# Kernel tuning notes

Hardware: AMD Instinct MI355X
Metric: run time of the kernel (lower is better)

## Reference

```python
import jax, jax.numpy as jnp
import numpy as np

NUM_NEG = 100
TEMP = 0.05
EPS = 1e-12  # matches F.normalize eps


def _l2norm(x):
    n = jnp.sqrt(jnp.sum(x * x, axis=-1, keepdims=True))
    return x / jnp.maximum(n, EPS)


def setup_inputs() -> dict:
    key = jax.random.key(0)
    k1, k2, k3, k4, k5, k6 = jax.random.split(key, 6)
    B, S, D = 1024, 50, 64
    NUM_ITEMS = 100000  # table has NUM_ITEMS+1 rows (row 0 = padding)
    N = B * S
    return {
        "output_embeddings": jax.random.normal(k1, (B, S, D), dtype=jnp.float32),
        "target_ids": jax.random.randint(k2, (B, S), 1, NUM_ITEMS + 1, dtype=jnp.int64)
                      if jax.config.jax_enable_x64 else
                      jax.random.randint(k2, (B, S), 1, NUM_ITEMS + 1).astype(jnp.int32),
        "all_item_embeddings": jax.random.normal(k3, (NUM_ITEMS + 1, D), dtype=jnp.float32),
        "supervision_weights": jax.random.uniform(k4, (B, S), dtype=jnp.float32),
        "neg_indices": jax.random.randint(k5, (N, NUM_NEG), 1, NUM_ITEMS + 1).astype(jnp.int32),
        "alt_neg_indices": jax.random.randint(k6, (N, NUM_NEG), 1, NUM_ITEMS + 1).astype(jnp.int32),
    }


def reference(output_embeddings, target_ids, all_item_embeddings,
              supervision_weights, neg_indices, alt_neg_indices):
    B, S, D = output_embeddings.shape
    flat_out = output_embeddings.reshape(-1, D)            # [N, D]
    flat_tgt = target_ids.reshape(-1)                       # [N]
    flat_w = supervision_weights.reshape(-1)                # [N]
    valid = flat_w > 0

    vo = _l2norm(flat_out)                                  # [N, D]
    items = _l2norm(all_item_embeddings)                    # [V, D]

    pos_e = items[flat_tgt]                                 # [N, D]
    pos_logit = jnp.sum(vo * pos_e, axis=1)                 # [N]

    # resample negatives that collide with the positive target
    neg = jnp.where(neg_indices != flat_tgt[:, None], neg_indices, alt_neg_indices)
    neg_e = items[neg]                                      # [N, K, D]
    neg_logits = jnp.einsum('nd,nkd->nk', vo, neg_e)        # [N, K]

    logits = jnp.concatenate([pos_logit[:, None], neg_logits], axis=1) / TEMP
    # cross-entropy with label 0 == logsumexp - positive logit
    loss_per = jax.nn.logsumexp(logits, axis=1) - logits[:, 0]

    wm = jnp.where(valid, flat_w, 0.0)
    return jnp.sum(loss_per * wm) / jnp.sum(wm)
```

## Files before the change

kernel.cpp:

```cpp
#include <hip/hip_runtime.h>


#define D_DIM 64
#define K_NEG 100
#define INV_TEMP 20.0f
#define MAX_LOGIT 20.0f
#define LOG2E 1.4426950408889634f
#define LN2 0.6931471805599453f

#define NBLK_MAIN 2048
#define NBLK_NORM 512
#define NT 7

typedef float fv2 __attribute__((ext_vector_type(2)));

__global__ __launch_bounds__(256) void normalize_kernel(
    const float* __restrict__ items, unsigned int* __restrict__ tab, int V) {
  const int lane = threadIdx.x & 63;
  const int wid  = threadIdx.x >> 6;
  const int g = lane >> 4, q = lane & 15;
  const int waveId = blockIdx.x * 4 + wid;
  const int nWaves = gridDim.x * 4;
  for (int base = waveId * 4; base < V; base += nWaves * 4) {
    const int r = base + g;
    const bool act = (r < V);
    float4 x = make_float4(0.f, 0.f, 0.f, 0.f);
    if (act) x = *reinterpret_cast<const float4*>(items + (size_t)r * D_DIM + q * 4);
    float ss = x.x * x.x + x.y * x.y + x.z * x.z + x.w * x.w;
    ss += __shfl_xor(ss, 1);
    ss += __shfl_xor(ss, 2);
    ss += __shfl_xor(ss, 4);
    ss += __shfl_xor(ss, 8);
    const float inv = 1.0f / fmaxf(sqrtf(ss), 1e-12f);
    if (act) {
      int u = 0;
      u = __builtin_amdgcn_cvt_pk_fp8_f32(x.x * inv, x.y * inv, u, false);
      u = __builtin_amdgcn_cvt_pk_fp8_f32(x.z * inv, x.w * inv, u, true);
      tab[(size_t)r * 16 + q] = (unsigned int)u;
    }
  }
}

__global__ __launch_bounds__(256, 4) void loss_kernel(
    const float* __restrict__ oe,
    const int*   __restrict__ tgt,
    const unsigned int* __restrict__ tab,
    const float* __restrict__ wgt,
    const int*   __restrict__ negi,
    const int*   __restrict__ alti,
    float2*      __restrict__ partials,
    int N) {
  const int lane = threadIdx.x & 63;
  const int wid  = threadIdx.x >> 6;
  const int g = lane >> 2, q = lane & 3;
  const int waveId = blockIdx.x * 4 + wid;
  const int nWaves = gridDim.x * 4;

  float num = 0.f, den = 0.f;

  int row = waveId;
  float4 a0, a1, a2, a3;
  int t_r = 0;
  float w = 0.f;
  int nj0 = 0, nj1 = 0, nj2 = 0, nj3 = 0, nj4 = 0, nj5 = 0, nj6 = 0;

  if (row < N) {
    const float* orow = oe + (size_t)row * D_DIM + q * 16;
    a0 = *reinterpret_cast<const float4*>(orow + 0);
    a1 = *reinterpret_cast<const float4*>(orow + 4);
    a2 = *reinterpret_cast<const float4*>(orow + 8);
    a3 = *reinterpret_cast<const float4*>(orow + 12);
    t_r = tgt[row];
    w = wgt[row];
    const int* nrow = negi + (size_t)row * K_NEG;
    if (g >= 1) nj0 = nrow[g - 1];
    nj1 = nrow[16 + g - 1];
    nj2 = nrow[32 + g - 1];
    nj3 = nrow[48 + g - 1];
    nj4 = nrow[64 + g - 1];
    nj5 = nrow[80 + g - 1];
    if (g <= 4) nj6 = nrow[96 + g - 1];
  }

  while (row < N) {
    const int nxt = row + nWaves;
    const int* __restrict__ arow = alti + (size_t)row * K_NEG;

    int idx[NT];
    {
      int v0 = (g == 0) ? t_r : nj0;
      if (g >= 1 && v0 == t_r) v0 = arow[g - 1];
      idx[0] = v0;
      int v1 = nj1; if (v1 == t_r) v1 = arow[16 + g - 1]; idx[1] = v1;
      int v2 = nj2; if (v2 == t_r) v2 = arow[32 + g - 1]; idx[2] = v2;
      int v3 = nj3; if (v3 == t_r) v3 = arow[48 + g - 1]; idx[3] = v3;
      int v4 = nj4; if (v4 == t_r) v4 = arow[64 + g - 1]; idx[4] = v4;
      int v5 = nj5; if (v5 == t_r) v5 = arow[80 + g - 1]; idx[5] = v5;
      int v6 = 0;
      if (g <= 4) { v6 = nj6; if (v6 == t_r) v6 = arow[96 + g - 1]; }
      idx[6] = v6;
    }

    uint4 rb[NT];
#pragma unroll
    for (int t = 0; t < NT; ++t)
      rb[t] = *reinterpret_cast<const uint4*>(tab + (size_t)idx[t] * 16 + q * 4);

    float4 b0, b1, b2, b3;
    int p_t = 0; float p_w = 0.f;
    int pn0 = 0, pn1 = 0, pn2 = 0, pn3 = 0, pn4 = 0, pn5 = 0, pn6 = 0;
    b0 = b1 = b2 = b3 = make_float4(0.f, 0.f, 0.f, 0.f);
    if (nxt < N) {
      const float* prow = oe + (size_t)nxt * D_DIM + q * 16;
      b0 = *reinterpret_cast<const float4*>(prow + 0);
      b1 = *reinterpret_cast<const float4*>(prow + 4);
      b2 = *reinterpret_cast<const float4*>(prow + 8);
      b3 = *reinterpret_cast<const float4*>(prow + 12);
      p_t = tgt[nxt];
      p_w = wgt[nxt];
      const int* nrow = negi + (size_t)nxt * K_NEG;
      if (g >= 1) pn0 = nrow[g - 1];
      pn1 = nrow[16 + g - 1];
      pn2 = nrow[32 + g - 1];
      pn3 = nrow[48 + g - 1];
      pn4 = nrow[64 + g - 1];
      pn5 = nrow[80 + g - 1];
      if (g <= 4) pn6 = nrow[96 + g - 1];
    }

    const fv2 qa0 = {a0.x, a0.y}, qa1 = {a0.z, a0.w};
    const fv2 qa2 = {a1.x, a1.y}, qa3 = {a1.z, a1.w};
    const fv2 qa4 = {a2.x, a2.y}, qa5 = {a2.z, a2.w};
    const fv2 qa6 = {a3.x, a3.y}, qa7 = {a3.z, a3.w};

    fv2 ss2 = qa0 * qa0;
    ss2 += qa1 * qa1;
    ss2 += qa2 * qa2;
    ss2 += qa3 * qa3;
    ss2 += qa4 * qa4;
    ss2 += qa5 * qa5;
    ss2 += qa6 * qa6;
    ss2 += qa7 * qa7;
    float ss = ss2[0] + ss2[1];
    ss += __shfl_xor(ss, 1);
    ss += __shfl_xor(ss, 2);
    const float inv_o = 1.0f / fmaxf(sqrtf(ss), 1e-12f);

    float sumexp = 0.f;
    float pos_logit = 0.f;

#pragma unroll
    for (int t = 0; t < NT; ++t) {
      const uint4 r = rb[t];
      fv2 acc;
      acc  = qa0 * __builtin_amdgcn_cvt_pk_f32_fp8((int)r.x, false);
      acc += qa1 * __builtin_amdgcn_cvt_pk_f32_fp8((int)r.x, true);
      acc += qa2 * __builtin_amdgcn_cvt_pk_f32_fp8((int)r.y, false);
      acc += qa3 * __builtin_amdgcn_cvt_pk_f32_fp8((int)r.y, true);
      acc += qa4 * __builtin_amdgcn_cvt_pk_f32_fp8((int)r.z, false);
      acc += qa5 * __builtin_amdgcn_cvt_pk_f32_fp8((int)r.z, true);
      acc += qa6 * __builtin_amdgcn_cvt_pk_f32_fp8((int)r.w, false);
      acc += qa7 * __builtin_amdgcn_cvt_pk_f32_fp8((int)r.w, true);
      float p = acc[0] + acc[1];
      p += __shfl_xor(p, 1);
      p += __shfl_xor(p, 2);
      const int j = t * 16 + g;
      if (q == 0 && j <= K_NEG) {
        const float logit = p * inv_o * INV_TEMP;
        sumexp += exp2f((logit - MAX_LOGIT) * LOG2E);
        if (j == 0) pos_logit = logit;
      }
    }
    sumexp += __shfl_xor(sumexp, 4);
    sumexp += __shfl_xor(sumexp, 8);
    sumexp += __shfl_xor(sumexp, 16);
    sumexp += __shfl_xor(sumexp, 32);
    if (lane == 0) {
      const float lse = log2f(sumexp) * LN2 + MAX_LOGIT;
      const float loss = lse - pos_logit;
      if (w > 0.f) {
        num += loss * w;
        den += w;
      }
    }

    a0 = b0; a1 = b1; a2 = b2; a3 = b3;
    t_r = p_t; w = p_w;
    nj0 = pn0; nj1 = pn1; nj2 = pn2; nj3 = pn3; nj4 = pn4; nj5 = pn5; nj6 = pn6;
    row = nxt;
  }

  __shared__ float2 red[4];
  if (lane == 0) red[wid] = make_float2(num, den);
  __syncthreads();
  if (threadIdx.x == 0) {
    float n = 0.f, d = 0.f;
#pragma unroll
    for (int i = 0; i < 4; ++i) { n += red[i].x; d += red[i].y; }
    partials[blockIdx.x] = make_float2(n, d);
  }
}

__global__ __launch_bounds__(256) void finish_kernel(
    const float2* __restrict__ partials, int nblk, float* __restrict__ out) {
  float num = 0.f, den = 0.f;
  for (int i = threadIdx.x; i < nblk; i += 256) {
    const float2 p = partials[i];
    num += p.x;
    den += p.y;
  }
#pragma unroll
  for (int m = 1; m < 64; m <<= 1) {
    num += __shfl_xor(num, m);
    den += __shfl_xor(den, m);
  }
  __shared__ float2 red[4];
  const int wid = threadIdx.x >> 6;
  const int lane = threadIdx.x & 63;
  if (lane == 0) red[wid] = make_float2(num, den);
  __syncthreads();
  if (threadIdx.x == 0) {
    float n = 0.f, d = 0.f;
#pragma unroll
    for (int i = 0; i < 4; ++i) { n += red[i].x; d += red[i].y; }
    out[0] = n / d;
  }
}

extern "C" void kernel_launch(void* const* d_in, const int* in_sizes, int n_in,
                              void* d_out, int out_size, void* d_ws, size_t ws_size,
                              hipStream_t stream) {
  const float* oe    = (const float*)d_in[0];
  const int*   tgt   = (const int*)  d_in[1];
  const float* items = (const float*)d_in[2];
  const float* wgt   = (const float*)d_in[3];
  const int*   negi  = (const int*)  d_in[4];
  const int*   alti  = (const int*)  d_in[5];

  const int N = in_sizes[0] / D_DIM;
  const int V = in_sizes[2] / D_DIM;

  unsigned int* tab = (unsigned int*)d_ws;
  size_t off = ((size_t)V * 16 * sizeof(unsigned int) + 255) & ~(size_t)255;
  float2* partials = (float2*)((char*)d_ws + off);

  normalize_kernel<<<NBLK_NORM, 256, 0, stream>>>(items, tab, V);
  loss_kernel<<<NBLK_MAIN, 256, 0, stream>>>(oe, tgt, tab, wgt, negi, alti,
                                             partials, N);
  finish_kernel<<<1, 256, 0, stream>>>(partials, NBLK_MAIN, (float*)d_out);
}
```

Before: 70.75 us.

## Switch to int8 quantized embeddings with sdot4 and one-lane-per-negative mapping

Replaces the fp8 item table with symmetric int8 quantization (scale 127) and also pre-quantizes the normalized output embeddings to int8 in a combined prepass kernel. The loss kernel now gives each lane a whole negative row (two per lane, 101 candidates) and computes dot products with packed int8 sdot4, dropping per-row norm computation, fp8 conversions and intra-row shuffles. Each lane now issues 64-byte gathers, and the prepass adds a write of the quantized output embeddings. Int8 rounding of both operands changes numerical accuracy relative to the fp8 version.

```diff
diff --git a/kernel.cpp b/kernel.cpp
--- a/kernel.cpp
+++ b/kernel.cpp
@@ -7,15 +7,40 @@
 #define MAX_LOGIT 20.0f
 #define LOG2E 1.4426950408889634f
 #define LN2 0.6931471805599453f
+#define MAXL2 28.853900817779268f
+#define MCONST (INV_TEMP / (127.0f * 127.0f))
+#define MC2 (MCONST * LOG2E)
 
 #define NBLK_MAIN 2048
-#define NBLK_NORM 512
-#define NT 7
-
-typedef float fv2 __attribute__((ext_vector_type(2)));
-
-__global__ __launch_bounds__(256) void normalize_kernel(
-    const float* __restrict__ items, unsigned int* __restrict__ tab, int V) {
+#define NBLK_QNT 1024
+
+typedef float fv4 __attribute__((ext_vector_type(4)));
+typedef unsigned int uv4 __attribute__((ext_vector_type(4)));
+
+__device__ __forceinline__ int DOT4(int a, int b, int c) {
+#if __has_builtin(__builtin_amdgcn_sdot4)
+  return __builtin_amdgcn_sdot4(a, b, c, false);
+#else
+  int r = c;
+#pragma unroll
+  for (int i = 0; i < 4; ++i)
+    r += (int)(signed char)(a >> (8 * i)) * (int)(signed char)(b >> (8 * i));
+  return r;
+#endif
+}
+
+__device__ __forceinline__ unsigned int pack8(const fv4 x, float s) {
+  const int b0 = (int)rintf(x.x * s) & 255;
+  const int b1 = (int)rintf(x.y * s) & 255;
+  const int b2 = (int)rintf(x.z * s) & 255;
+  const int b3 = (int)rintf(x.w * s) & 255;
+  return (unsigned)b0 | ((unsigned)b1 << 8) | ((unsigned)b2 << 16) |
+         ((unsigned)b3 << 24);
+}
+
+__global__ __launch_bounds__(256) void quantize_kernel(
+    const float* __restrict__ items, unsigned int* __restrict__ tab8, int V,
+    const float* __restrict__ oe, unsigned int* __restrict__ q8, int N) {
   const int lane = threadIdx.x & 63;
   const int wid  = threadIdx.x >> 6;
   const int g = lane >> 4, q = lane & 15;
@@ -24,179 +49,149 @@
   for (int base = waveId * 4; base < V; base += nWaves * 4) {
     const int r = base + g;
     const bool act = (r < V);
-    float4 x = make_float4(0.f, 0.f, 0.f, 0.f);
-    if (act) x = *reinterpret_cast<const float4*>(items + (size_t)r * D_DIM + q * 4);
+    fv4 x = {0.f, 0.f, 0.f, 0.f};
+    if (act) x = *reinterpret_cast<const fv4*>(items + (size_t)r * D_DIM + q * 4);
     float ss = x.x * x.x + x.y * x.y + x.z * x.z + x.w * x.w;
     ss += __shfl_xor(ss, 1);
     ss += __shfl_xor(ss, 2);
     ss += __shfl_xor(ss, 4);
     ss += __shfl_xor(ss, 8);
-    const float inv = 1.0f / fmaxf(sqrtf(ss), 1e-12f);
-    if (act) {
-      int u = 0;
-      u = __builtin_amdgcn_cvt_pk_fp8_f32(x.x * inv, x.y * inv, u, false);
-      u = __builtin_amdgcn_cvt_pk_fp8_f32(x.z * inv, x.w * inv, u, true);
-      tab[(size_t)r * 16 + q] = (unsigned int)u;
-    }
-  }
-}
-
-__global__ __launch_bounds__(256, 4) void loss_kernel(
-    const float* __restrict__ oe,
+    const float s = 127.0f / fmaxf(sqrtf(ss), 1e-12f);
+    if (act) tab8[(size_t)r * 16 + q] = pack8(x, s);
+  }
+  for (int base = waveId * 4; base < N; base += nWaves * 4) {
+    const int r = base + g;
+    const bool act = (r < N);
+    fv4 x = {0.f, 0.f, 0.f, 0.f};
+    if (act) x = *reinterpret_cast<const fv4*>(oe + (size_t)r * D_DIM + q * 4);
+    float ss = x.x * x.x + x.y * x.y + x.z * x.z + x.w * x.w;
+    ss += __shfl_xor(ss, 1);
+    ss += __shfl_xor(ss, 2);
+    ss += __shfl_xor(ss, 4);
+    ss += __shfl_xor(ss, 8);
+    const float s = 127.0f / fmaxf(sqrtf(ss), 1e-12f);
+    if (act) q8[(size_t)r * 16 + q] = pack8(x, s);
+  }
+}
+
+__global__ __launch_bounds__(256) void loss_kernel(
+    const unsigned int* __restrict__ q8,
     const int*   __restrict__ tgt,
-    const unsigned int* __restrict__ tab,
+    const unsigned int* __restrict__ tab8,
     const float* __restrict__ wgt,
     const int*   __restrict__ negi,
     const int*   __restrict__ alti,
     float2*      __restrict__ partials,
     int N) {
+  __shared__ float2 s_red[4];
   const int lane = threadIdx.x & 63;
   const int wid  = threadIdx.x >> 6;
-  const int g = lane >> 2, q = lane & 3;
   const int waveId = blockIdx.x * 4 + wid;
   const int nWaves = gridDim.x * 4;
+  const bool v1ok = (lane <= K_NEG - 64);
 
   float num = 0.f, den = 0.f;
 
   int row = waveId;
-  float4 a0, a1, a2, a3;
-  int t_r = 0;
+  int t_r = 0, n0 = 0, n1 = 0;
   float w = 0.f;
-  int nj0 = 0, nj1 = 0, nj2 = 0, nj3 = 0, nj4 = 0, nj5 = 0, nj6 = 0;
-
   if (row < N) {
-    const float* orow = oe + (size_t)row * D_DIM + q * 16;
-    a0 = *reinterpret_cast<const float4*>(orow + 0);
-    a1 = *reinterpret_cast<const float4*>(orow + 4);
-    a2 = *reinterpret_cast<const float4*>(orow + 8);
-    a3 = *reinterpret_cast<const float4*>(orow + 12);
     t_r = tgt[row];
     w = wgt[row];
-    const int* nrow = negi + (size_t)row * K_NEG;
-    if (g >= 1) nj0 = nrow[g - 1];
-    nj1 = nrow[16 + g - 1];
-    nj2 = nrow[32 + g - 1];
-    nj3 = nrow[48 + g - 1];
-    nj4 = nrow[64 + g - 1];
-    nj5 = nrow[80 + g - 1];
-    if (g <= 4) nj6 = nrow[96 + g - 1];
+    const int* nr = negi + (size_t)row * K_NEG;
+    if (lane >= 1) n0 = nr[lane - 1];
+    if (v1ok) n1 = nr[63 + lane];
   }
 
   while (row < N) {
     const int nxt = row + nWaves;
-    const int* __restrict__ arow = alti + (size_t)row * K_NEG;
-
-    int idx[NT];
-    {
-      int v0 = (g == 0) ? t_r : nj0;
-      if (g >= 1 && v0 == t_r) v0 = arow[g - 1];
-      idx[0] = v0;
-      int v1 = nj1; if (v1 == t_r) v1 = arow[16 + g - 1]; idx[1] = v1;
-      int v2 = nj2; if (v2 == t_r) v2 = arow[32 + g - 1]; idx[2] = v2;
-      int v3 = nj3; if (v3 == t_r) v3 = arow[48 + g - 1]; idx[3] = v3;
-      int v4 = nj4; if (v4 == t_r) v4 = arow[64 + g - 1]; idx[4] = v4;
-      int v5 = nj5; if (v5 == t_r) v5 = arow[80 + g - 1]; idx[5] = v5;
-      int v6 = 0;
-      if (g <= 4) { v6 = nj6; if (v6 == t_r) v6 = arow[96 + g - 1]; }
-      idx[6] = v6;
-    }
-
-    uint4 rb[NT];
-#pragma unroll
-    for (int t = 0; t < NT; ++t)
-      rb[t] = *reinterpret_cast<const uint4*>(tab + (size_t)idx[t] * 16 + q * 4);
-
-    float4 b0, b1, b2, b3;
-    int p_t = 0; float p_w = 0.f;
-    int pn0 = 0, pn1 = 0, pn2 = 0, pn3 = 0, pn4 = 0, pn5 = 0, pn6 = 0;
-    b0 = b1 = b2 = b3 = make_float4(0.f, 0.f, 0.f, 0.f);
+
+    const int* ar = alti + (size_t)row * K_NEG;
+    int i0 = (lane == 0) ? t_r : n0;
+    if (lane >= 1 && i0 == t_r) i0 = ar[lane - 1];
+    int i1 = v1ok ? n1 : 0;
+    if (v1ok && i1 == t_r) i1 = ar[63 + lane];
+
+    const uv4* t0 = reinterpret_cast<const uv4*>(tab8 + ((unsigned)i0 << 4));
+    const uv4* t1 = reinterpret_cast<const uv4*>(tab8 + ((unsigned)i1 << 4));
+    const uv4 a0 = t0[0], a1 = t0[1], a2 = t0[2], a3 = t0[3];
+    const uv4 b0 = t1[0], b1 = t1[1], b2 = t1[2], b3 = t1[3];
+    const uv4* qp = reinterpret_cast<const uv4*>(q8 + (size_t)row * 16);
+    const uv4 q0 = qp[0], q1 = qp[1], q2 = qp[2], q3 = qp[3];
+
+    int p_t = 0, pn0 = 0, pn1 = 0;
+    float p_w = 0.f;
     if (nxt < N) {
-      const float* prow = oe + (size_t)nxt * D_DIM + q * 16;
-      b0 = *reinterpret_cast<const float4*>(prow + 0);
-      b1 = *reinterpret_cast<const float4*>(prow + 4);
-      b2 = *reinterpret_cast<const float4*>(prow + 8);
-      b3 = *reinterpret_cast<const float4*>(prow + 12);
       p_t = tgt[nxt];
       p_w = wgt[nxt];
-      const int* nrow = negi + (size_t)nxt * K_NEG;
-      if (g >= 1) pn0 = nrow[g - 1];
-      pn1 = nrow[16 + g - 1];
-      pn2 = nrow[32 + g - 1];
-      pn3 = nrow[48 + g - 1];
-      pn4 = nrow[64 + g - 1];
-      pn5 = nrow[80 + g - 1];
-      if (g <= 4) pn6 = nrow[96 + g - 1];
+      const int* nr = negi + (size_t)nxt * K_NEG;
+      if (lane >= 1) pn0 = __builtin_nontemporal_load(nr + lane - 1);
+      if (v1ok) pn1 = __builtin_nontemporal_load(nr + 63 + lane);
     }
 
-    const fv2 qa0 = {a0.x, a0.y}, qa1 = {a0.z, a0.w};
-    const fv2 qa2 = {a1.x, a1.y}, qa3 = {a1.z, a1.w};
-    const fv2 qa4 = {a2.x, a2.y}, qa5 = {a2.z, a2.w};
-    const fv2 qa6 = {a3.x, a3.y}, qa7 = {a3.z, a3.w};
-
-    fv2 ss2 = qa0 * qa0;
-    ss2 += qa1 * qa1;
-    ss2 += qa2 * qa2;
-    ss2 += qa3 * qa3;
-    ss2 += qa4 * qa4;
-    ss2 += qa5 * qa5;
-    ss2 += qa6 * qa6;
-    ss2 += qa7 * qa7;
-    float ss = ss2[0] + ss2[1];
-    ss += __shfl_xor(ss, 1);
-    ss += __shfl_xor(ss, 2);
-    const float inv_o = 1.0f / fmaxf(sqrtf(ss), 1e-12f);
-
-    float sumexp = 0.f;
-    float pos_logit = 0.f;
-
-#pragma unroll
-    for (int t = 0; t < NT; ++t) {
-      const uint4 r = rb[t];
-      fv2 acc;
-      acc  = qa0 * __builtin_amdgcn_cvt_pk_f32_fp8((int)r.x, false);
-      acc += qa1 * __builtin_amdgcn_cvt_pk_f32_fp8((int)r.x, true);
-      acc += qa2 * __builtin_amdgcn_cvt_pk_f32_fp8((int)r.y, false);
-      acc += qa3 * __builtin_amdgcn_cvt_pk_f32_fp8((int)r.y, true);
-      acc += qa4 * __builtin_amdgcn_cvt_pk_f32_fp8((int)r.z, false);
-      acc += qa5 * __builtin_amdgcn_cvt_pk_f32_fp8((int)r.z, true);
-      acc += qa6 * __builtin_amdgcn_cvt_pk_f32_fp8((int)r.w, false);
-      acc += qa7 * __builtin_amdgcn_cvt_pk_f32_fp8((int)r.w, true);
-      float p = acc[0] + acc[1];
-      p += __shfl_xor(p, 1);
-      p += __shfl_xor(p, 2);
-      const int j = t * 16 + g;
-      if (q == 0 && j <= K_NEG) {
-        const float logit = p * inv_o * INV_TEMP;
-        sumexp += exp2f((logit - MAX_LOGIT) * LOG2E);
-        if (j == 0) pos_logit = logit;
-      }
-    }
-    sumexp += __shfl_xor(sumexp, 4);
-    sumexp += __shfl_xor(sumexp, 8);
-    sumexp += __shfl_xor(sumexp, 16);
-    sumexp += __shfl_xor(sumexp, 32);
+    int d0 = 0, d1 = 0;
+    d0 = DOT4((int)a0.x, (int)q0.x, d0);
+    d1 = DOT4((int)b0.x, (int)q0.x, d1);
+    d0 = DOT4((int)a0.y, (int)q0.y, d0);
+    d1 = DOT4((int)b0.y, (int)q0.y, d1);
+    d0 = DOT4((int)a0.z, (int)q0.z, d0);
+    d1 = DOT4((int)b0.z, (int)q0.z, d1);
+    d0 = DOT4((int)a0.w, (int)q0.w, d0);
+    d1 = DOT4((int)b0.w, (int)q0.w, d1);
+    d0 = DOT4((int)a1.x, (int)q1.x, d0);
+    d1 = DOT4((int)b1.x, (int)q1.x, d1);
+    d0 = DOT4((int)a1.y, (int)q1.y, d0);
+    d1 = DOT4((int)b1.y, (int)q1.y, d1);
+    d0 = DOT4((int)a1.z, (int)q1.z, d0);
+    d1 = DOT4((int)b1.z, (int)q1.z, d1);
+    d0 = DOT4((int)a1.w, (int)q1.w, d0);
+    d1 = DOT4((int)b1.w, (int)q1.w, d1);
+    d0 = DOT4((int)a2.x, (int)q2.x, d0);
+    d1 = DOT4((int)b2.x, (int)q2.x, d1);
+    d0 = DOT4((int)a2.y, (int)q2.y, d0);
+    d1 = DOT4((int)b2.y, (int)q2.y, d1);
+    d0 = DOT4((int)a2.z, (int)q2.z, d0);
+    d1 = DOT4((int)b2.z, (int)q2.z, d1);
+    d0 = DOT4((int)a2.w, (int)q2.w, d0);
+    d1 = DOT4((int)b2.w, (int)q2.w, d1);
+    d0 = DOT4((int)a3.x, (int)q3.x, d0);
+    d1 = DOT4((int)b3.x, (int)q3.x, d1);
+    d0 = DOT4((int)a3.y, (int)q3.y, d0);
+    d1 = DOT4((int)b3.y, (int)q3.y, d1);
+    d0 = DOT4((int)a3.z, (int)q3.z, d0);
+    d1 = DOT4((int)b3.z, (int)q3.z, d1);
+    d0 = DOT4((int)a3.w, (int)q3.w, d0);
+    d1 = DOT4((int)b3.w, (int)q3.w, d1);
+
+    float e = exp2f(fmaf((float)d0, MC2, -MAXL2));
+    if (v1ok) e += exp2f(fmaf((float)d1, MC2, -MAXL2));
+
+    e += __shfl_xor(e, 1);
+    e += __shfl_xor(e, 2);
+    e += __shfl_xor(e, 4);
+    e += __shfl_xor(e, 8);
+    e += __shfl_xor(e, 16);
+    e += __shfl_xor(e, 32);
     if (lane == 0) {
-      const float lse = log2f(sumexp) * LN2 + MAX_LOGIT;
-      const float loss = lse - pos_logit;
+      const float pos = (float)d0 * MCONST;
+      const float lse = log2f(e) * LN2 + MAX_LOGIT;
+      const float loss = lse - pos;
       if (w > 0.f) {
         num += loss * w;
         den += w;
       }
     }
 
-    a0 = b0; a1 = b1; a2 = b2; a3 = b3;
-    t_r = p_t; w = p_w;
-    nj0 = pn0; nj1 = pn1; nj2 = pn2; nj3 = pn3; nj4 = pn4; nj5 = pn5; nj6 = pn6;
+    t_r = p_t; n0 = pn0; n1 = pn1; w = p_w;
     row = nxt;
   }
 
-  __shared__ float2 red[4];
-  if (lane == 0) red[wid] = make_float2(num, den);
+  if (lane == 0) s_red[wid] = make_float2(num, den);
   __syncthreads();
   if (threadIdx.x == 0) {
     float n = 0.f, d = 0.f;
 #pragma unroll
-    for (int i = 0; i < 4; ++i) { n += red[i].x; d += red[i].y; }
+    for (int i = 0; i < 4; ++i) { n += s_red[i].x; d += s_red[i].y; }
     partials[blockIdx.x] = make_float2(n, d);
   }
 }
@@ -240,12 +235,14 @@
   const int N = in_sizes[0] / D_DIM;
   const int V = in_sizes[2] / D_DIM;
 
-  unsigned int* tab = (unsigned int*)d_ws;
-  size_t off = ((size_t)V * 16 * sizeof(unsigned int) + 255) & ~(size_t)255;
-  float2* partials = (float2*)((char*)d_ws + off);
-
-  normalize_kernel<<<NBLK_NORM, 256, 0, stream>>>(items, tab, V);
-  loss_kernel<<<NBLK_MAIN, 256, 0, stream>>>(oe, tgt, tab, wgt, negi, alti,
+  unsigned int* tab8 = (unsigned int*)d_ws;
+  size_t off = ((size_t)V * 64 + 255) & ~(size_t)255;
+  unsigned int* q8 = (unsigned int*)((char*)d_ws + off);
+  size_t off2 = (off + (size_t)N * 64 + 255) & ~(size_t)255;
+  float2* partials = (float2*)((char*)d_ws + off2);
+
+  quantize_kernel<<<NBLK_QNT, 256, 0, stream>>>(items, tab8, V, oe, q8, N);
+  loss_kernel<<<NBLK_MAIN, 256, 0, stream>>>(q8, tgt, tab8, wgt, negi, alti,
                                              partials, N);
   finish_kernel<<<1, 256, 0, stream>>>(partials, NBLK_MAIN, (float*)d_out);
 }
```

Measured after the change: 72.73 us. +2.8%, slower.
